# Optimization experiments

Measured on AMD Instinct MI355X. Metric: run time of the kernel, lower is better.

## Reference

```python
import jax, jax.numpy as jnp
import numpy as np

B, S, D = 16, 2048, 128


def setup_inputs() -> dict:
    key = jax.random.key(0)
    kq, kk, kv, km = jax.random.split(key, 4)
    q = jax.random.normal(kq, (B, S, D), dtype=jnp.float32)
    k = jax.random.normal(kk, (B, S, D), dtype=jnp.float32)
    v = jax.random.normal(kv, (B, S, D), dtype=jnp.float32)
    mask = jax.random.randint(km, (B, S, S), 0, 2, dtype=jnp.int32)
    return {"q": q, "k": k, "v": v, "mask": mask}


def softmax_one(x):
    # repo's softmax_one: subtract max, denominator is 1 + sum(exp)
    x = x - jnp.max(x, axis=-1, keepdims=True)
    e = jnp.exp(x)
    return e / (1.0 + jnp.sum(e, axis=-1, keepdims=True))


def reference(q, k, v, mask):
    d_k = k.shape[-1]
    zero = jnp.zeros((q.shape[0], 1, d_k), dtype=q.dtype)
    # prepend zero 'sink' key/value token along the sequence axis
    k1 = jnp.concatenate([zero, k], axis=1)          # [B, S+1, D]
    v1 = jnp.concatenate([zero, v], axis=1)          # [B, S+1, D]
    scores = jnp.einsum('bqd,bkd->bqk', q, k1) / np.sqrt(d_k)  # [B, S, S+1]
    # F.pad(mask, (1, 0)) pads sink column with 0 -> sink score masked
    m = jnp.pad(mask, ((0, 0), (0, 0), (1, 0)))
    scores = jnp.where(m == 0, jnp.float32(-1e9), scores)
    p_attn = softmax_one(scores)                     # [B, S, S+1]
    out = jnp.einsum('bqk,bkd->bqd', p_attn, v1)     # [B, S, D]
    return (out, p_attn)
```

## Files before the change

kernel.cpp:

```cpp
#include <hip/hip_runtime.h>
#include <hip/hip_bf16.h>

typedef __attribute__((ext_vector_type(8))) __bf16 bf16x8;
typedef __attribute__((ext_vector_type(4))) __bf16 bf16x4;
typedef __attribute__((ext_vector_type(4))) float  f32x4;
typedef float f32x4u __attribute__((ext_vector_type(4), aligned(4)));

#define NB 16
#define NS 2048
#define ND 128
#define QT 64
#define KT 64
#define NKT (NS / KT)
#define SCALE 0.08838834764831845f

__device__ __forceinline__ bf16x8 ld8_256(const __bf16* base, int row, int byteInRow) {
    int off = row * 256 + (byteInRow ^ ((row & 7) << 4));
    return *reinterpret_cast<const bf16x8*>(reinterpret_cast<const char*>(base) + off);
}
__device__ __forceinline__ bf16x8 ld8_128(const __bf16* base, int row, int byteInRow) {
    int off = row * 128 + (byteInRow ^ ((row & 7) << 4));
    return *reinterpret_cast<const bf16x8*>(reinterpret_cast<const char*>(base) + off);
}

__global__ __launch_bounds__(256) void conv_qk(const float* __restrict__ q,
                                               const float* __restrict__ k,
                                               __bf16* __restrict__ qb,
                                               __bf16* __restrict__ kb) {
    size_t i = (size_t)blockIdx.x * 256 + threadIdx.x;
    const float4* qs = (const float4*)q;
    const float4* ks = (const float4*)k;
    float4 a = qs[2 * i], b = qs[2 * i + 1];
    bf16x8 o;
    o[0] = (__bf16)(a.x * SCALE); o[1] = (__bf16)(a.y * SCALE);
    o[2] = (__bf16)(a.z * SCALE); o[3] = (__bf16)(a.w * SCALE);
    o[4] = (__bf16)(b.x * SCALE); o[5] = (__bf16)(b.y * SCALE);
    o[6] = (__bf16)(b.z * SCALE); o[7] = (__bf16)(b.w * SCALE);
    *(bf16x8*)&qb[i * 8] = o;
    a = ks[2 * i]; b = ks[2 * i + 1];
    o[0] = (__bf16)a.x; o[1] = (__bf16)a.y; o[2] = (__bf16)a.z; o[3] = (__bf16)a.w;
    o[4] = (__bf16)b.x; o[5] = (__bf16)b.y; o[6] = (__bf16)b.z; o[7] = (__bf16)b.w;
    *(bf16x8*)&kb[i * 8] = o;
}

__global__ __launch_bounds__(256) void conv_vt(const float* __restrict__ v,
                                               __bf16* __restrict__ vt) {
    __shared__ __bf16 tile[128 * 128];
    const int b = blockIdx.x >> 4, st = blockIdx.x & 15;
    const int s0 = st * 128, t = threadIdx.x;
    const int rlane = t >> 5, cv = (t & 31) * 4;
    #pragma unroll
    for (int it = 0; it < 16; ++it) {
        int s = rlane + it * 8;
        float4 f = *(const float4*)(v + ((size_t)b * NS + s0 + s) * ND + cv);
        bf16x4 h;
        h[0] = (__bf16)f.x; h[1] = (__bf16)f.y; h[2] = (__bf16)f.z; h[3] = (__bf16)f.w;
        *(bf16x4*)&tile[s * 128 + (cv ^ (s & 60))] = h;
    }
    __syncthreads();
    #pragma unroll
    for (int it = 0; it < 16; ++it) {
        int d = rlane + it * 8;
        bf16x4 o;
        #pragma unroll
        for (int e = 0; e < 4; ++e)
            o[e] = tile[(cv + e) * 128 + (d ^ ((cv + e) & 60))];
        *(bf16x4*)&vt[((size_t)b * ND + d) * NS + s0 + cv] = o;
    }
}

__global__ __launch_bounds__(256, 2) void qa_main(
    const __bf16* __restrict__ qb, const __bf16* __restrict__ kb,
    const __bf16* __restrict__ vtb, const int* __restrict__ mg,
    float* __restrict__ outg, float* __restrict__ pg)
{
    __shared__ unsigned short bmt[NKT * 256];
    __shared__ __align__(16) __bf16 Ps[4][16 * KT];

    const int bid = blockIdx.x;
    const int lb  = (bid & 7) * 64 + (bid >> 3);
    const int b   = lb >> 5;
    const int q0  = (lb & 31) * QT;
    const int t   = threadIdx.x;
    const int w   = t >> 6;
    const int l   = t & 63;
    const int l15 = l & 15;
    const int g   = l >> 4;
    const int myrow = w * 16 + l15;

    const __bf16* kbB  = kb  + (size_t)b * NS * ND;
    const __bf16* vtbB = vtb + (size_t)b * ND * NS;
    const int*    mrow = mg  + (size_t)(b * NS + q0 + myrow) * NS;

    if (t < QT) pg[(size_t)(b * NS + q0 + t) * (size_t)(NS + 1)] = 0.0f;

    bf16x8 qf[4];
    {
        const __bf16* qrow = qb + (size_t)(b * NS + q0 + myrow) * ND;
        #pragma unroll
        for (int kc = 0; kc < 4; ++kc)
            qf[kc] = *(const bf16x8*)(qrow + kc * 32 + g * 8);
    }

    bf16x8 kf[16];
    f32x4  acc[4];

    auto loadK = [&](int k0) {
        #pragma unroll
        for (int c = 0; c < 4; ++c)
            #pragma unroll
            for (int kc = 0; kc < 4; ++kc)
                kf[c * 4 + kc] = *(const bf16x8*)(kbB + (size_t)(k0 + c * 16 + l15) * ND + kc * 32 + g * 8);
    };
    auto qk = [&]() {
        #pragma unroll
        for (int c = 0; c < 4; ++c) {
            f32x4 z = {0.f, 0.f, 0.f, 0.f}; acc[c] = z;
            #pragma unroll
            for (int kc = 0; kc < 4; ++kc)
                acc[c] = __builtin_amdgcn_mfma_f32_16x16x32_bf16(kf[c * 4 + kc], qf[kc], acc[c], 0, 0, 0);
        }
    };

    float mrun = -1e9f, srun = 0.0f;
    int4 mA[4], mB[4];

    auto stepA = [&](int kt, const int4* mcur, int4* mnxt) {
        qk();
        const int kn = kt + 1;
        if (kn < NKT) {
            loadK(kn * KT);
            #pragma unroll
            for (int c = 0; c < 4; ++c)
                mnxt[c] = *(const int4*)(mrow + kn * KT + c * 16 + g * 4);
        }
        float sv[16]; unsigned bits = 0;
        #pragma unroll
        for (int c = 0; c < 4; ++c) {
            int mm[4] = {mcur[c].x, mcur[c].y, mcur[c].z, mcur[c].w};
            #pragma unroll
            for (int r = 0; r < 4; ++r) {
                bool on = mm[r] != 0;
                sv[c * 4 + r] = on ? acc[c][r] : -1e30f;
                bits |= on ? (1u << (c * 4 + r)) : 0u;
            }
        }
        float x0 = fmaxf(fmaxf(sv[0], sv[1]),  fmaxf(sv[2], sv[3]));
        float x1 = fmaxf(fmaxf(sv[4], sv[5]),  fmaxf(sv[6], sv[7]));
        float x2 = fmaxf(fmaxf(sv[8], sv[9]),  fmaxf(sv[10], sv[11]));
        float x3 = fmaxf(fmaxf(sv[12], sv[13]), fmaxf(sv[14], sv[15]));
        float mx = fmaxf(fmaxf(x0, x1), fmaxf(x2, x3));
        mx = fmaxf(mx, __shfl_xor(mx, 16));
        mx = fmaxf(mx, __shfl_xor(mx, 32));
        float mnew = fmaxf(mrun, mx);
        float e[16];
        #pragma unroll
        for (int i = 0; i < 16; ++i) e[i] = __expf(sv[i] - mnew);
        float s0 = (e[0] + e[1]) + (e[2] + e[3]);
        float s1 = (e[4] + e[5]) + (e[6] + e[7]);
        float s2 = (e[8] + e[9]) + (e[10] + e[11]);
        float s3 = (e[12] + e[13]) + (e[14] + e[15]);
        float ps = (s0 + s1) + (s2 + s3);
        ps += __shfl_xor(ps, 16);
        ps += __shfl_xor(ps, 32);
        srun = srun * __expf(mrun - mnew) + ps;
        mrun = mnew;
        bmt[kt * 256 + t] = (unsigned short)bits;
    };

    loadK(0);
    #pragma unroll
    for (int c = 0; c < 4; ++c) mA[c] = *(const int4*)(mrow + c * 16 + g * 4);
    for (int kt = 0; kt < NKT; kt += 2) {
        stepA(kt,     mA, mB);
        stepA(kt + 1, mB, mA);
    }

    const float inv = 1.0f / (1.0f + srun);

    f32x4 oacc[8];
    #pragma unroll
    for (int cf = 0; cf < 8; ++cf) { f32x4 z = {0.f, 0.f, 0.f, 0.f}; oacc[cf] = z; }

    bf16x8 vf[16];
    auto loadV = [&](int k0) {
        #pragma unroll
        for (int kc = 0; kc < 2; ++kc)
            #pragma unroll
            for (int cf = 0; cf < 8; ++cf)
                vf[kc * 8 + cf] = *(const bf16x8*)(vtbB + (size_t)(cf * 16 + l15) * NS + k0 + kc * 32 + g * 8);
    };

    loadK(0);
    loadV(0);
    const size_t prow = (size_t)(b * NS + q0 + myrow) * (size_t)(NS + 1);
    __bf16* Psw = Ps[w];

    for (int kt = 0; kt < NKT; ++kt) {
        const int k0 = kt * KT;
        qk();
        if (kt + 1 < NKT) loadK(k0 + KT);

        unsigned bits = bmt[kt * 256 + t];
        #pragma unroll
        for (int c = 0; c < 4; ++c) {
            f32x4 pv; bf16x4 pb;
            #pragma unroll
            for (int r = 0; r < 4; ++r) {
                bool on = (bits >> (c * 4 + r)) & 1u;
                float p = on ? __expf(acc[c][r] - mrun) * inv : 0.0f;
                pv[r] = p; pb[r] = (__bf16)p;
            }
            *(f32x4u*)&pg[prow + 1 + k0 + c * 16 + g * 4] = pv;
            int off = l15 * 128 + ((c * 32 + g * 8) ^ ((l15 & 7) << 4));
            *(bf16x4*)((char*)Psw + off) = pb;
        }

        #pragma unroll
        for (int kc = 0; kc < 2; ++kc) {
            bf16x8 af = ld8_128(Psw, l15, kc * 64 + g * 16);
            #pragma unroll
            for (int cf = 0; cf < 8; ++cf)
                oacc[cf] = __builtin_amdgcn_mfma_f32_16x16x32_bf16(af, vf[kc * 8 + cf], oacc[cf], 0, 0, 0);
        }
        if (kt + 1 < NKT) loadV(k0 + KT);
    }

    #pragma unroll
    for (int cf = 0; cf < 8; ++cf)
        #pragma unroll
        for (int r = 0; r < 4; ++r)
            outg[(size_t)(b * NS + q0 + w * 16 + g * 4 + r) * ND + cf * 16 + l15] = oacc[cf][r];
}

__device__ __forceinline__ void stage_rm(__bf16* dst, const float* src, int t) {
    int row = t >> 2, cg = t & 3;
    const float4* s4 = reinterpret_cast<const float4*>(src + (size_t)row * ND) + cg * 8;
    #pragma unroll
    for (int j = 0; j < 8; ++j) {
        float4 f = s4[j];
        bf16x4 h;
        h[0] = (__bf16)f.x; h[1] = (__bf16)f.y; h[2] = (__bf16)f.z; h[3] = (__bf16)f.w;
        int off = (cg * 64 + j * 8) ^ ((row & 7) << 4);
        *reinterpret_cast<bf16x4*>(reinterpret_cast<char*>(dst) + row * 256 + off) = h;
    }
}

__global__ __launch_bounds__(256, 2) void qa_fused_fb(
    const float* __restrict__ qg, const float* __restrict__ kg,
    const float* __restrict__ vg, const int* __restrict__ mg,
    float* __restrict__ outg, float* __restrict__ pg)
{
    __shared__ __bf16 Qs[QT * ND];
    __shared__ __bf16 Ks[KT * ND];
    __shared__ __bf16 Vt[ND * KT];
    __shared__ __bf16 Psf[4 * 16 * KT];
    __shared__ unsigned int bmf[QT][64];

    const int bid = blockIdx.x;
    const int lb  = (bid & 7) * 64 + (bid >> 3);
    const int b   = lb >> 5;
    const int q0  = (lb & 31) * QT;
    const int t   = threadIdx.x;
    const int w   = t >> 6;
    const int l   = t & 63;
    const int l15 = l & 15;
    const int g   = l >> 4;

    stage_rm(Qs, qg + ((size_t)b * NS + q0) * ND, t);
    if (t < QT) pg[((size_t)b * NS + q0 + t) * (size_t)(NS + 1)] = 0.0f;
    __syncthreads();

    bf16x8 qf[4];
    const int arow = w * 16 + l15;
    #pragma unroll
    for (int kc = 0; kc < 4; ++kc) qf[kc] = ld8_256(Qs, arow, kc * 64 + g * 16);

    float mrun[4], srun[4];
    #pragma unroll
    for (int r = 0; r < 4; ++r) { mrun[r] = -1e9f; srun[r] = 0.0f; }

    for (int kt = 0; kt < NKT; ++kt) {
        const int k0 = kt * KT;
        __syncthreads();
        stage_rm(Ks, kg + ((size_t)b * NS + k0) * ND, t);
        #pragma unroll 4
        for (int i = 0; i < 16; ++i) {
            int row = w * 16 + i;
            int mv = mg[((size_t)b * NS + (q0 + row)) * NS + k0 + l];
            unsigned long long bal = __ballot(mv != 0);
            if (l == 0) {
                bmf[row][2 * kt]     = (unsigned)bal;
                bmf[row][2 * kt + 1] = (unsigned)(bal >> 32);
            }
        }
        __syncthreads();

        f32x4 acc[4];
        #pragma unroll
        for (int c = 0; c < 4; ++c) {
            f32x4 z = {0.f, 0.f, 0.f, 0.f};
            acc[c] = z;
            #pragma unroll
            for (int kc = 0; kc < 4; ++kc) {
                bf16x8 bf = ld8_256(Ks, c * 16 + l15, kc * 64 + g * 16);
                acc[c] = __builtin_amdgcn_mfma_f32_16x16x32_bf16(qf[kc], bf, acc[c], 0, 0, 0);
            }
        }

        #pragma unroll
        for (int r = 0; r < 4; ++r) {
            const int row = w * 16 + g * 4 + r;
            const unsigned w0 = bmf[row][2 * kt], w1 = bmf[row][2 * kt + 1];
            float sv[4], tmax = -1e9f;
            #pragma unroll
            for (int c = 0; c < 4; ++c) {
                int cb = c * 16 + l15;
                unsigned word = (c < 2) ? w0 : w1;
                bool on = (word >> (cb & 31)) & 1u;
                float s = on ? acc[c][r] * SCALE : -1e9f;
                sv[c] = s;
                tmax = fmaxf(tmax, s);
            }
            #pragma unroll
            for (int d = 1; d < 16; d <<= 1) tmax = fmaxf(tmax, __shfl_xor(tmax, d));
            float mnew = fmaxf(mrun[r], tmax);
            float corr = __expf(mrun[r] - mnew);
            float ps = 0.f;
            #pragma unroll
            for (int c = 0; c < 4; ++c) ps += __expf(sv[c] - mnew);
            #pragma unroll
            for (int d = 1; d < 16; d <<= 1) ps += __shfl_xor(ps, d);
            srun[r] = srun[r] * corr + ps;
            mrun[r] = mnew;
        }
    }

    float inv[4];
    #pragma unroll
    for (int r = 0; r < 4; ++r) inv[r] = 1.0f / (1.0f + srun[r]);

    f32x4 oacc[8];
    #pragma unroll
    for (int cf = 0; cf < 8; ++cf) { f32x4 z = {0.f,0.f,0.f,0.f}; oacc[cf] = z; }

    __bf16* Psw = Psf + w * (16 * KT);

    for (int kt = 0; kt < NKT; ++kt) {
        const int k0 = kt * KT;
        __syncthreads();
        stage_rm(Ks, kg + ((size_t)b * NS + k0) * ND, t);
        {
            int kk = t >> 2, dg = t & 3;
            const float4* s4 = reinterpret_cast<const float4*>(vg + ((size_t)b * NS + k0 + kk) * ND) + dg * 8;
            #pragma unroll
            for (int j = 0; j < 8; ++j) {
                float4 f = s4[j];
                int d0 = dg * 32 + j * 4;
                float fv[4] = {f.x, f.y, f.z, f.w};
                #pragma unroll
                for (int e = 0; e < 4; ++e) {
                    int d = d0 + e;
                    int off = d * 128 + ((kk * 2) ^ ((d & 7) << 4));
                    *reinterpret_cast<__bf16*>(reinterpret_cast<char*>(Vt) + off) = (__bf16)fv[e];
                }
            }
        }
        __syncthreads();

        f32x4 acc[4];
        #pragma unroll
        for (int c = 0; c < 4; ++c) {
            f32x4 z = {0.f, 0.f, 0.f, 0.f};
            acc[c] = z;
            #pragma unroll
            for (int kc = 0; kc < 4; ++kc) {
                bf16x8 bf = ld8_256(Ks, c * 16 + l15, kc * 64 + g * 16);
                acc[c] = __builtin_amdgcn_mfma_f32_16x16x32_bf16(qf[kc], bf, acc[c], 0, 0, 0);
            }
        }

        #pragma unroll
        for (int r = 0; r < 4; ++r) {
            const int row16 = g * 4 + r;
            const int row = w * 16 + row16;
            const unsigned w0 = bmf[row][2 * kt], w1 = bmf[row][2 * kt + 1];
            const size_t prowf = ((size_t)b * NS + q0 + row) * (size_t)(NS + 1);
            #pragma unroll
            for (int c = 0; c < 4; ++c) {
                int cb = c * 16 + l15;
                unsigned word = (c < 2) ? w0 : w1;
                bool on = (word >> (cb & 31)) & 1u;
                float p = on ? __expf(acc[c][r] * SCALE - mrun[r]) * inv[r] : 0.0f;
                pg[prowf + 1 + k0 + cb] = p;
                int off = row16 * 128 + ((cb * 2) ^ ((row16 & 7) << 4));
                *reinterpret_cast<__bf16*>(reinterpret_cast<char*>(Psw) + off) = (__bf16)p;
            }
        }

        #pragma unroll
        for (int kc = 0; kc < 2; ++kc) {
            bf16x8 af = ld8_128(Psw, l15, kc * 64 + g * 16);
            #pragma unroll
            for (int cf = 0; cf < 8; ++cf) {
                bf16x8 vfr = ld8_128(Vt, cf * 16 + l15, kc * 64 + g * 16);
                oacc[cf] = __builtin_amdgcn_mfma_f32_16x16x32_bf16(af, vfr, oacc[cf], 0, 0, 0);
            }
        }
    }

    #pragma unroll
    for (int cf = 0; cf < 8; ++cf)
        #pragma unroll
        for (int r = 0; r < 4; ++r)
            outg[((size_t)b * NS + q0 + w * 16 + g * 4 + r) * ND + cf * 16 + l15] = oacc[cf][r];
}

extern "C" void kernel_launch(void* const* d_in, const int* in_sizes, int n_in,
                              void* d_out, int out_size, void* d_ws, size_t ws_size,
                              hipStream_t stream) {
    const float* q = (const float*)d_in[0];
    const float* k = (const float*)d_in[1];
    const float* v = (const float*)d_in[2];
    const int*  mk = (const int*)d_in[3];
    float* out = (float*)d_out;
    float* p   = out + (size_t)NB * NS * ND;

    const size_t elems = (size_t)NB * NS * ND;
    const size_t need  = elems * 2 * 3;

    if (ws_size >= need) {
        __bf16* qb = (__bf16*)d_ws;
        __bf16* kb = qb + elems;
        __bf16* vt = kb + elems;
        conv_qk<<<dim3((unsigned)(elems / 8 / 256)), dim3(256), 0, stream>>>(q, k, qb, kb);
        conv_vt<<<dim3(NB * 16), dim3(256), 0, stream>>>(v, vt);
        qa_main<<<dim3(NB * (NS / QT)), dim3(256), 0, stream>>>(qb, kb, vt, mk, out, p);
    } else {
        qa_fused_fb<<<dim3(NB * (NS / QT)), dim3(256), 0, stream>>>(q, k, v, mk, out, p);
    }
}
```

Before: 778.3 us.

## Stage K and V tiles into LDS via async global_load_lds triple buffering

Replaces the per-wave register loads of K and V fragments with cooperative global-to-LDS direct loads into three rotating XOR-swizzled shared buffers. Explicit vmcnt waits and block barriers order the pipeline in both the stats pass and the output pass. The goal is to stop each of the four waves from separately loading the same K/V tiles from global memory, and to cut register pressure by reading fragments from LDS. In exchange it adds about 48KB of LDS per block, which may limit occupancy at 2 blocks/CU, plus barrier overhead. The hand-written vmcnt counts must also line up with the interleaved mask and P stores.

Result: faster. 631.9 us (-18.8%).

```diff
diff --git a/kernel.cpp b/kernel.cpp
--- a/kernel.cpp
+++ b/kernel.cpp
@@ -14,6 +14,12 @@
 #define NKT (NS / KT)
 #define SCALE 0.08838834764831845f
 
+#define VMW12() asm volatile("s_waitcnt vmcnt(12)" ::: "memory")
+#define VMW8()  asm volatile("s_waitcnt vmcnt(8)"  ::: "memory")
+#define VMW4()  asm volatile("s_waitcnt vmcnt(4)"  ::: "memory")
+#define SCHED0() __builtin_amdgcn_sched_barrier(0)
+#define SBAR()  __builtin_amdgcn_s_barrier()
+
 __device__ __forceinline__ bf16x8 ld8_256(const __bf16* base, int row, int byteInRow) {
     int off = row * 256 + (byteInRow ^ ((row & 7) << 4));
     return *reinterpret_cast<const bf16x8*>(reinterpret_cast<const char*>(base) + off);
@@ -21,6 +27,11 @@
 __device__ __forceinline__ bf16x8 ld8_128(const __bf16* base, int row, int byteInRow) {
     int off = row * 128 + (byteInRow ^ ((row & 7) << 4));
     return *reinterpret_cast<const bf16x8*>(reinterpret_cast<const char*>(base) + off);
+}
+__device__ __forceinline__ void glds16(const void* g, void* l) {
+    __builtin_amdgcn_global_load_lds(
+        (const __attribute__((address_space(1))) unsigned int*)g,
+        (__attribute__((address_space(3))) unsigned int*)l, 16, 0, 0);
 }
 
 __global__ __launch_bounds__(256) void conv_qk(const float* __restrict__ q,
@@ -74,6 +85,7 @@
     const __bf16* __restrict__ vtb, const int* __restrict__ mg,
     float* __restrict__ outg, float* __restrict__ pg)
 {
+    __shared__ __align__(16) char bufs[3][KT * ND * 2];
     __shared__ unsigned short bmt[NKT * 256];
     __shared__ __align__(16) __bf16 Ps[4][16 * KT];
 
@@ -83,9 +95,8 @@
     const int q0  = (lb & 31) * QT;
     const int t   = threadIdx.x;
     const int w   = t >> 6;
-    const int l   = t & 63;
-    const int l15 = l & 15;
-    const int g   = l >> 4;
+    const int l15 = t & 15;
+    const int g   = (t & 63) >> 4;
     const int myrow = w * 16 + l15;
 
     const __bf16* kbB  = kb  + (size_t)b * NS * ND;
@@ -102,37 +113,50 @@
             qf[kc] = *(const bf16x8*)(qrow + kc * 32 + g * 8);
     }
 
-    bf16x8 kf[16];
-    f32x4  acc[4];
-
-    auto loadK = [&](int k0) {
-        #pragma unroll
-        for (int c = 0; c < 4; ++c)
-            #pragma unroll
-            for (int kc = 0; kc < 4; ++kc)
-                kf[c * 4 + kc] = *(const bf16x8*)(kbB + (size_t)(k0 + c * 16 + l15) * ND + kc * 32 + g * 8);
+    auto stageK = [&](char* buf, int k0) {
+        #pragma unroll
+        for (int i = 0; i < 4; ++i) {
+            int c = i * 256 + t;
+            int row = c >> 4, pc = c & 15, lc = pc ^ (row & 7);
+            glds16(kbB + (size_t)(k0 + row) * ND + lc * 8, buf + c * 16);
+        }
     };
-    auto qk = [&]() {
-        #pragma unroll
-        for (int c = 0; c < 4; ++c) {
-            f32x4 z = {0.f, 0.f, 0.f, 0.f}; acc[c] = z;
-            #pragma unroll
-            for (int kc = 0; kc < 4; ++kc)
-                acc[c] = __builtin_amdgcn_mfma_f32_16x16x32_bf16(kf[c * 4 + kc], qf[kc], acc[c], 0, 0, 0);
+    auto stageV = [&](char* buf, int k0) {
+        #pragma unroll
+        for (int i = 0; i < 4; ++i) {
+            int c = i * 256 + t;
+            int d = c >> 3, pc = c & 7, lc = pc ^ (d & 7);
+            glds16(vtbB + (size_t)d * NS + k0 + lc * 8, buf + c * 16);
         }
     };
 
     float mrun = -1e9f, srun = 0.0f;
     int4 mA[4], mB[4];
 
+    stageK(bufs[0], 0);
+    stageK(bufs[1], KT);
+    #pragma unroll
+    for (int c = 0; c < 4; ++c) mA[c] = *(const int4*)(mrow + c * 16 + g * 4);
+    VMW8();
+    SCHED0(); SBAR(); SCHED0();
+
     auto stepA = [&](int kt, const int4* mcur, int4* mnxt) {
-        qk();
-        const int kn = kt + 1;
-        if (kn < NKT) {
-            loadK(kn * KT);
+        if (kt + 2 < NKT) stageK(bufs[(kt + 2) % 3], (kt + 2) * KT);
+        if (kt + 1 < NKT) {
             #pragma unroll
             for (int c = 0; c < 4; ++c)
-                mnxt[c] = *(const int4*)(mrow + kn * KT + c * 16 + g * 4);
+                mnxt[c] = *(const int4*)(mrow + (kt + 1) * KT + c * 16 + g * 4);
+        }
+        const __bf16* Kbuf = (const __bf16*)bufs[kt % 3];
+        f32x4 acc[4];
+        #pragma unroll
+        for (int c = 0; c < 4; ++c) {
+            f32x4 z = {0.f, 0.f, 0.f, 0.f}; acc[c] = z;
+            #pragma unroll
+            for (int kc = 0; kc < 4; ++kc) {
+                bf16x8 kf = ld8_256(Kbuf, c * 16 + l15, kc * 64 + g * 16);
+                acc[c] = __builtin_amdgcn_mfma_f32_16x16x32_bf16(kf, qf[kc], acc[c], 0, 0, 0);
+            }
         }
         float sv[16]; unsigned bits = 0;
         #pragma unroll
@@ -156,21 +180,21 @@
         float e[16];
         #pragma unroll
         for (int i = 0; i < 16; ++i) e[i] = __expf(sv[i] - mnew);
-        float s0 = (e[0] + e[1]) + (e[2] + e[3]);
-        float s1 = (e[4] + e[5]) + (e[6] + e[7]);
-        float s2 = (e[8] + e[9]) + (e[10] + e[11]);
-        float s3 = (e[12] + e[13]) + (e[14] + e[15]);
-        float ps = (s0 + s1) + (s2 + s3);
+        float p0 = (e[0] + e[1]) + (e[2] + e[3]);
+        float p1 = (e[4] + e[5]) + (e[6] + e[7]);
+        float p2 = (e[8] + e[9]) + (e[10] + e[11]);
+        float p3 = (e[12] + e[13]) + (e[14] + e[15]);
+        float ps = (p0 + p1) + (p2 + p3);
         ps += __shfl_xor(ps, 16);
         ps += __shfl_xor(ps, 32);
         srun = srun * __expf(mrun - mnew) + ps;
         mrun = mnew;
         bmt[kt * 256 + t] = (unsigned short)bits;
+        if (kt <= NKT - 3)      { VMW12(); }
+        else if (kt == NKT - 2) { VMW8();  }
+        SCHED0(); SBAR(); SCHED0();
     };
 
-    loadK(0);
-    #pragma unroll
-    for (int c = 0; c < 4; ++c) mA[c] = *(const int4*)(mrow + c * 16 + g * 4);
     for (int kt = 0; kt < NKT; kt += 2) {
         stepA(kt,     mA, mB);
         stepA(kt + 1, mB, mA);
@@ -182,24 +206,30 @@
     #pragma unroll
     for (int cf = 0; cf < 8; ++cf) { f32x4 z = {0.f, 0.f, 0.f, 0.f}; oacc[cf] = z; }
 
-    bf16x8 vf[16];
-    auto loadV = [&](int k0) {
-        #pragma unroll
-        for (int kc = 0; kc < 2; ++kc)
-            #pragma unroll
-            for (int cf = 0; cf < 8; ++cf)
-                vf[kc * 8 + cf] = *(const bf16x8*)(vtbB + (size_t)(cf * 16 + l15) * NS + k0 + kc * 32 + g * 8);
-    };
-
-    loadK(0);
-    loadV(0);
+    int iA = 0, iB = 1, iC = 2;
+    stageK(bufs[0], 0);
+    stageV(bufs[1], 0);
+    VMW4();
+    SCHED0(); SBAR(); SCHED0();
+
     const size_t prow = (size_t)(b * NS + q0 + myrow) * (size_t)(NS + 1);
     __bf16* Psw = Ps[w];
 
     for (int kt = 0; kt < NKT; ++kt) {
         const int k0 = kt * KT;
-        qk();
-        if (kt + 1 < NKT) loadK(k0 + KT);
+        if (kt + 1 < NKT) stageK(bufs[iC], k0 + KT);
+
+        const __bf16* Kbuf = (const __bf16*)bufs[iA];
+        f32x4 acc[4];
+        #pragma unroll
+        for (int c = 0; c < 4; ++c) {
+            f32x4 z = {0.f, 0.f, 0.f, 0.f}; acc[c] = z;
+            #pragma unroll
+            for (int kc = 0; kc < 4; ++kc) {
+                bf16x8 kf = ld8_256(Kbuf, c * 16 + l15, kc * 64 + g * 16);
+                acc[c] = __builtin_amdgcn_mfma_f32_16x16x32_bf16(kf, qf[kc], acc[c], 0, 0, 0);
+            }
+        }
 
         unsigned bits = bmt[kt * 256 + t];
         #pragma unroll
@@ -216,14 +246,27 @@
             *(bf16x4*)((char*)Psw + off) = pb;
         }
 
+        if (kt < NKT - 1) { VMW8(); } else { VMW4(); }
+        SCHED0(); SBAR(); SCHED0();
+
+        if (kt + 1 < NKT) stageV(bufs[iA], k0 + KT);
+
+        const __bf16* Vbuf = (const __bf16*)bufs[iB];
         #pragma unroll
         for (int kc = 0; kc < 2; ++kc) {
             bf16x8 af = ld8_128(Psw, l15, kc * 64 + g * 16);
             #pragma unroll
-            for (int cf = 0; cf < 8; ++cf)
-                oacc[cf] = __builtin_amdgcn_mfma_f32_16x16x32_bf16(af, vf[kc * 8 + cf], oacc[cf], 0, 0, 0);
-        }
-        if (kt + 1 < NKT) loadV(k0 + KT);
+            for (int cf = 0; cf < 8; ++cf) {
+                bf16x8 vf = ld8_128(Vbuf, cf * 16 + l15, kc * 64 + g * 16);
+                oacc[cf] = __builtin_amdgcn_mfma_f32_16x16x32_bf16(af, vf, oacc[cf], 0, 0, 0);
+            }
+        }
+
+        if (kt < NKT - 1) { VMW8(); }
+        SCHED0(); SBAR(); SCHED0();
+
+        int nA = iC, nB = iA, nC = iB;
+        iA = nA; iB = nB; iC = nC;
     }
 
     #pragma unroll
```
